# Performance work log

Measured on AMD Instinct MI355X. Metric: run time of the kernel, lower is better.

Reference implementation:

```python
import jax, jax.numpy as jnp
import numpy as np

B, N, C = 1, 256, 128        # batch, n_res, norm_channel
H, AC = 4, 32                # num_head, attention_channel


def setup_inputs() -> dict:
    key = jax.random.key(0)
    ks = jax.random.split(key, 9)
    s = 0.02
    return {
        "act": jax.random.normal(ks[0], (B, N, N, C), jnp.float32),
        "mask": jnp.ones((B, N, N), jnp.float32),
        "ln_g": jnp.ones((C,), jnp.float32),
        "ln_b": jnp.zeros((C,), jnp.float32),
        "wq": (jax.random.normal(ks[1], (C, H * AC), jnp.float32) * s),
        "wk": (jax.random.normal(ks[2], (C, H * AC), jnp.float32) * s),
        "wv": (jax.random.normal(ks[3], (C, H * AC), jnp.float32) * s),
        "w2d": (jax.random.normal(ks[4], (C, H), jnp.float32) * s),
        "wg": (jax.random.normal(ks[5], (C, H * AC), jnp.float32) * s),
        "bg": jnp.zeros((H * AC,), jnp.float32),
        "wo": (jax.random.normal(ks[6], (H * AC, C), jnp.float32) * s),
        "bo": jnp.zeros((C,), jnp.float32),
    }


def reference(act, mask, ln_g, ln_b, wq, wk, wv, w2d, wg, bg, wo, bo):
    eps = 1e-5
    mu = jnp.mean(act, axis=-1, keepdims=True)
    var = jnp.mean(jnp.square(act - mu), axis=-1, keepdims=True)
    a = (act - mu) * jax.lax.rsqrt(var + eps) * ln_g + ln_b  # LayerNorm

    b_, m_, i_, _ = a.shape
    q = (a @ wq).reshape(b_, m_, i_, H, AC)
    k = (a @ wk).reshape(b_, m_, i_, H, AC)
    v = (a @ wv).reshape(b_, m_, i_, H, AC)

    factor = 1.0 / np.sqrt(AC).astype(np.float32)
    # mask bias: [b, m, 1, 1, j]
    bias = (1e9 * (mask - 1.0))[:, :, None, None, :]
    aff = jnp.einsum('bmihc,bmjhc->bmhij', q * factor, k) + bias

    # pair bias: [b, h, i, j], broadcast over m (torch trailing-dim broadcast, b=1)
    nb = jnp.einsum('bijc,ch->bhij', a, w2d)
    weights = jax.nn.softmax(aff + nb[:, None], axis=-1)  # [b,m,h,i,j]

    g = jax.nn.sigmoid(a @ wg + bg).reshape(b_, m_, i_, H, AC)
    out = jnp.einsum('bmhqk,bmkhc->bmqhc', weights, v) * g  # [b,m,q,h,c]
    return out.reshape(b_, m_, i_, H * AC) @ wo + bo
```

## Files before the change

### kernel.cpp

```cpp
#include <hip/hip_runtime.h>
#include <hip/hip_fp16.h>
#include <math.h>


#define NRES 256
#define CCH  128
#define NROWS (NRES * NRES)
#define FACTOR 0.17677669529663687f
#define LOG2E  1.44269504088896341f

typedef __attribute__((ext_vector_type(8))) __bf16 bf16x8;
typedef __attribute__((ext_vector_type(4))) float f32x4;
typedef __attribute__((ext_vector_type(4))) short s16x4;

__device__ __forceinline__ f32x4 mfma16(bf16x8 a, bf16x8 b, f32x4 c) {
    return __builtin_amdgcn_mfma_f32_16x16x32_bf16(a, b, c, 0, 0, 0);
}
__device__ __forceinline__ f32x4 mfma16x16(s16x4 a, s16x4 b, f32x4 c) {
    return __builtin_amdgcn_mfma_f32_16x16x16bf16_1k(a, b, c, 0, 0, 0);
}

union PK4 { __bf16 b[4]; uint2 u2; s16x4 s4; };

__device__ __forceinline__ void hilo(float x, __bf16& h, __bf16& l) {
    h = (__bf16)x;
    l = (__bf16)(x - (float)h);
}

__global__ __launch_bounds__(256) void pre_kernel(
    const float* __restrict__ act, const float* __restrict__ ln_g,
    const float* __restrict__ ln_b, const float* __restrict__ w2d,
    const float* __restrict__ wq, const float* __restrict__ wk,
    const float* __restrict__ wv, const float* __restrict__ wg,
    const float* __restrict__ wo,
    __bf16* __restrict__ wph, __bf16* __restrict__ wo16h,
    __bf16* __restrict__ wo16l,
    float* __restrict__ nbP, __bf16* __restrict__ aLN)
{
    const int t = threadIdx.x;
    if (blockIdx.x >= 2048) {
        const int gid = (blockIdx.x - 2048) * 256 + t;
        const int wid = gid >> 11;
        const int rem = gid & 2047;
        const int lane = rem & 63;
        const int l15 = lane & 15, quad = lane >> 4;
        if (wid < 4) {
            const int nstrip = rem >> 8;
            const int kf = (rem >> 6) & 3;
            const float* W = (wid == 0) ? wq : (wid == 1) ? wk :
                             (wid == 2) ? wv : wg;
            const float scale = (wid == 0) ? FACTOR * LOG2E : 1.0f;
            bf16x8 hb;
            #pragma unroll
            for (int e = 0; e < 8; ++e) {
                int k = kf * 32 + quad * 8 + e;
                int n = nstrip * 16 + l15;
                hb[e] = (__bf16)(W[k * CCH + n] * scale);
            }
            *(bf16x8*)&wph[(size_t)gid * 8] = hb;
        } else {
            const int nstrip = rem >> 8;
            const int kcp = (rem >> 6) & 3;
            #pragma unroll
            for (int sub = 0; sub < 2; ++sub) {
                const int kc = kcp * 2 + sub;
                PK4 hh, ll;
                #pragma unroll
                for (int e = 0; e < 4; ++e) {
                    int k = kc * 16 + quad * 4 + e;
                    int n = nstrip * 16 + l15;
                    __bf16 h, l; hilo(wo[k * CCH + n], h, l);
                    hh.b[e] = h; ll.b[e] = l;
                }
                const int fo = ((nstrip * 8 + kc) * 64 + lane) * 4;
                *(uint2*)&wo16h[fo] = hh.u2;
                *(uint2*)&wo16l[fo] = ll.u2;
            }
        }
        return;
    }
    const int ridx = t >> 3, g = t & 7;
    const int grow = blockIdx.x * 32 + ridx;
    const float* __restrict__ xp = act + (size_t)grow * CCH + g * 16;
    float4 x4[4];
    #pragma unroll
    for (int c = 0; c < 4; ++c) x4[c] = *(const float4*)(xp + c * 4);
    float s = 0.f, sq = 0.f;
    #pragma unroll
    for (int c = 0; c < 4; ++c) {
        s  += (x4[c].x + x4[c].y) + (x4[c].z + x4[c].w);
        sq += x4[c].x * x4[c].x + x4[c].y * x4[c].y +
              x4[c].z * x4[c].z + x4[c].w * x4[c].w;
    }
    #pragma unroll
    for (int o = 1; o <= 4; o <<= 1) {
        s  += __shfl_xor(s, o, 64);
        sq += __shfl_xor(sq, o, 64);
    }
    float mu  = s * (1.0f / CCH);
    float var = fmaf(sq, 1.0f / CCH, -mu * mu);
    float rs  = rsqrtf(var + 1e-5f);
    float av[16];
    #pragma unroll
    for (int c = 0; c < 4; ++c) {
        float4 g4 = *(const float4*)&ln_g[g * 16 + c * 4];
        float4 b4 = *(const float4*)&ln_b[g * 16 + c * 4];
        float* xv = (float*)&x4[c];
        float* gv = (float*)&g4;
        float* bv = (float*)&b4;
        #pragma unroll
        for (int e = 0; e < 4; ++e)
            av[c * 4 + e] = fmaf((xv[e] - mu) * rs, gv[e], bv[e]);
    }
    bf16x8 o1, o2;
    #pragma unroll
    for (int e = 0; e < 8; ++e) {
        o1[e] = (__bf16)av[e];
        o2[e] = (__bf16)av[8 + e];
    }
    *(bf16x8*)&aLN[(size_t)grow * CCH + g * 16] = o1;
    *(bf16x8*)&aLN[(size_t)grow * CCH + g * 16 + 8] = o2;

    float nb[4] = {0.f, 0.f, 0.f, 0.f};
    const float4* __restrict__ w2d4 = (const float4*)w2d;
    #pragma unroll
    for (int c = 0; c < 16; ++c) {
        float4 wv = w2d4[g * 16 + c];
        nb[0] = fmaf(av[c], wv.x, nb[0]);
        nb[1] = fmaf(av[c], wv.y, nb[1]);
        nb[2] = fmaf(av[c], wv.z, nb[2]);
        nb[3] = fmaf(av[c], wv.w, nb[3]);
    }
    #pragma unroll
    for (int o = 1; o <= 4; o <<= 1)
        #pragma unroll
        for (int hh = 0; hh < 4; ++hh)
            nb[hh] += __shfl_xor(nb[hh], o, 64);
    if (g == 0) {
        const int i = grow >> 8, j = grow & 255;
        #pragma unroll
        for (int hh = 0; hh < 4; ++hh) {
            size_t f = ((size_t)hh << 14) + ((size_t)(i >> 4) << 10) +
                       ((size_t)(j >> 4) << 6) + ((size_t)((j >> 2) & 3) << 4) +
                       (i & 15);
            nbP[f * 4 + (j & 3)] = nb[hh] * LOG2E;
        }
    }
}

__device__ __forceinline__ void proj16(const bf16x8* A0,
    const __bf16* __restrict__ Bh, int lane, f32x4* acc)
{
    #pragma unroll
    for (int n = 0; n < 8; ++n) acc[n] = (f32x4){0.f, 0.f, 0.f, 0.f};
    #pragma unroll
    for (int kf = 0; kf < 4; ++kf)
        #pragma unroll
        for (int n = 0; n < 8; ++n) {
            bf16x8 bh = *(const bf16x8*)&Bh[(size_t)((n * 4 + kf) * 64 + lane) * 8];
            acc[n] = mfma16(A0[kf], bh, acc[n]);
        }
}

__global__ __launch_bounds__(1024) void mega_kernel(
    const __bf16* __restrict__ aLN, const __bf16* __restrict__ wph,
    const __bf16* __restrict__ wo16h, const __bf16* __restrict__ wo16l,
    const float* __restrict__ bg, const float* __restrict__ mask,
    const float* __restrict__ nbP, const float* __restrict__ bo,
    float* __restrict__ out)
{
    __shared__ __align__(16) char smem[138240];
    const int t = threadIdx.x, w = t >> 6, lane = t & 63;
    const int l15 = lane & 15, quad = lane >> 4;
    const int m = blockIdx.x;
    __bf16* const Kl = (__bf16*)smem;
    __bf16* const aH = (__bf16*)(smem + w * 4352);
    __bf16* const VT = (__bf16*)(smem + 69632);
    float*  const biasrow = (float*)(smem + 137216);

    if (t < 256)
        biasrow[t] = fmaf(1.442695e9f, mask[m * NRES + t] - 1.0f, -4.0f * LOG2E);

    bf16x8 A0[4];
    {
        const __bf16* __restrict__ ap =
            aLN + ((size_t)m * NRES + w * 16 + l15) * CCH;
        #pragma unroll
        for (int kf = 0; kf < 4; ++kf)
            A0[kf] = *(const bf16x8*)&ap[kf * 32 + quad * 8];
    }

    f32x4 acc[8];
    bf16x8 Qh[4];
    uint2  greg[4][2];

    proj16(A0, wph, lane, acc);
    {
        __bf16* const sth = aH;
        #pragma unroll
        for (int n = 0; n < 8; ++n)
            #pragma unroll
            for (int r = 0; r < 4; ++r)
                sth[(quad * 4 + r) * 136 + n * 16 + l15] = (__bf16)acc[n][r];
        #pragma unroll
        for (int h = 0; h < 4; ++h)
            Qh[h] = *(const bf16x8*)&sth[l15 * 136 + h * 32 + quad * 8];
    }

    proj16(A0, wph + 3 * 16384, lane, acc);
    {
        __half* const sthH = (__half*)aH;
        #pragma unroll
        for (int n = 0; n < 8; ++n)
            #pragma unroll
            for (int r = 0; r < 4; ++r) {
                float v = acc[n][r] + bg[n * 16 + l15];
                sthH[(quad * 4 + r) * 136 + n * 16 + l15] =
                    (__half)(1.0f / (1.0f + __expf(-v)));
            }
        #pragma unroll
        for (int h = 0; h < 4; ++h)
            #pragma unroll
            for (int c = 0; c < 2; ++c)
                greg[h][c] =
                    *(const uint2*)&sthH[l15 * 136 + h * 32 + c * 16 + quad * 4];
    }

    proj16(A0, wph + 1 * 16384, lane, acc);
    #pragma unroll
    for (int n = 0; n < 8; ++n)
        #pragma unroll
        for (int r = 0; r < 4; ++r)
            aH[(quad * 4 + r) * 136 + n * 16 + l15] = (__bf16)acc[n][r];

    proj16(A0, wph + 2 * 16384, lane, acc);
    {
        const int jcol = w * 16 + quad * 4;
        #pragma unroll
        for (int n = 0; n < 8; ++n) {
            PK4 pv;
            #pragma unroll
            for (int r = 0; r < 4; ++r) pv.b[r] = (__bf16)acc[n][r];
            *(uint2*)&VT[(n * 16 + l15) * 264 + jcol] = pv.u2;
        }
    }

    __syncthreads();

    PK4 ovh[4][2], ovl[4][2];
    #pragma unroll
    for (int h = 0; h < 4; ++h) {
        f32x4 O[2];
        O[0] = (f32x4){0.f, 0.f, 0.f, 0.f};
        O[1] = (f32x4){0.f, 0.f, 0.f, 0.f};
        float ls = 0.f;
        const int nbbase = (h * 16384 + w * 1024 + quad * 16 + l15) * 4;
        #pragma unroll 1
        for (int jb = 0; jb < NRES; jb += 64) {
            bf16x8 Kh[4];
            #pragma unroll
            for (int u = 0; u < 4; ++u)
                Kh[u] = *(const bf16x8*)&Kl[(jb + u * 16 + l15) * 136 +
                                            h * 32 + quad * 8];
            PK4 Vf[2][4];
            #pragma unroll
            for (int c = 0; c < 2; ++c)
                #pragma unroll
                for (int u = 0; u < 4; ++u)
                    Vf[c][u].u2 = *(const uint2*)&VT[
                        (h * 32 + c * 16 + l15) * 264 + jb + u * 16 + quad * 4];
            float4 nb4[4];
            #pragma unroll
            for (int u = 0; u < 4; ++u)
                nb4[u] = *(const float4*)(nbP + nbbase +
                                          (((jb >> 4) + u) << 8));
            f32x4 S[4];
            #pragma unroll
            for (int u = 0; u < 4; ++u) {
                S[u] = (f32x4){0.f, 0.f, 0.f, 0.f};
                S[u] = mfma16(Kh[u], Qh[h], S[u]);
            }
            PK4 PJ[4];
            #pragma unroll
            for (int u = 0; u < 4; ++u) {
                float4 mb = *(const float4*)&biasrow[jb + u * 16 + quad * 4];
                float p0 = exp2f(S[u][0] + nb4[u].x + mb.x);
                float p1 = exp2f(S[u][1] + nb4[u].y + mb.y);
                float p2 = exp2f(S[u][2] + nb4[u].z + mb.z);
                float p3 = exp2f(S[u][3] + nb4[u].w + mb.w);
                ls += (p0 + p1) + (p2 + p3);
                PJ[u].b[0] = (__bf16)p0; PJ[u].b[1] = (__bf16)p1;
                PJ[u].b[2] = (__bf16)p2; PJ[u].b[3] = (__bf16)p3;
            }
            #pragma unroll
            for (int c = 0; c < 2; ++c)
                #pragma unroll
                for (int u = 0; u < 4; ++u)
                    O[c] = mfma16x16(Vf[c][u].s4, PJ[u].s4, O[c]);
        }
        ls += __shfl_xor(ls, 16, 64);
        ls += __shfl_xor(ls, 32, 64);
        float inv = 1.0f / ls;
        #pragma unroll
        for (int c = 0; c < 2; ++c) {
            const __half* gh = (const __half*)&greg[h][c];
            #pragma unroll
            for (int r = 0; r < 4; ++r) {
                float v = O[c][r] * inv * (float)gh[r];
                __bf16 hb; __bf16 lb; hilo(v, hb, lb);
                ovh[h][c].b[r] = hb; ovl[h][c].b[r] = lb;
            }
        }
    }

    {
        #pragma unroll
        for (int n = 0; n < 8; ++n) acc[n] = (f32x4){0.f, 0.f, 0.f, 0.f};
        #pragma unroll
        for (int kc = 0; kc < 8; ++kc) {
            const int h = kc >> 1, c = kc & 1;
            s16x4 Ah = ovh[h][c].s4;
            s16x4 Al = ovl[h][c].s4;
            #pragma unroll
            for (int n = 0; n < 8; ++n) {
                const int fo = ((n * 8 + kc) * 64 + lane) * 4;
                PK4 bh, bl;
                bh.u2 = *(const uint2*)&wo16h[fo];
                bl.u2 = *(const uint2*)&wo16l[fo];
                acc[n] = mfma16x16(Ah, bh.s4, acc[n]);
                acc[n] = mfma16x16(Ah, bl.s4, acc[n]);
                acc[n] = mfma16x16(Al, bh.s4, acc[n]);
            }
        }

        const size_t rbase = (size_t)m * NRES + w * 16;
        #pragma unroll
        for (int n = 0; n < 8; ++n) {
            float b = bo[n * 16 + l15];
            #pragma unroll
            for (int r = 0; r < 4; ++r)
                out[(rbase + quad * 4 + r) * CCH + n * 16 + l15] = acc[n][r] + b;
        }
    }
}

extern "C" void kernel_launch(void* const* d_in, const int* in_sizes, int n_in,
                              void* d_out, int out_size, void* d_ws, size_t ws_size,
                              hipStream_t stream)
{
    const float* act  = (const float*)d_in[0];
    const float* mask = (const float*)d_in[1];
    const float* ln_g = (const float*)d_in[2];
    const float* ln_b = (const float*)d_in[3];
    const float* wq   = (const float*)d_in[4];
    const float* wk   = (const float*)d_in[5];
    const float* wv   = (const float*)d_in[6];
    const float* w2d  = (const float*)d_in[7];
    const float* wg   = (const float*)d_in[8];
    const float* bg   = (const float*)d_in[9];
    const float* wo   = (const float*)d_in[10];
    const float* bo   = (const float*)d_in[11];
    float* out = (float*)d_out;

    float* nbP    = (float*)d_ws;
    __bf16* wph   = (__bf16*)(nbP + 4 * NROWS);
    __bf16* wo16h = wph + 4 * 16384;
    __bf16* wo16l = wo16h + 16384;
    __bf16* aLN   = wo16l + 16384;

    pre_kernel<<<2088, 256, 0, stream>>>(
        act, ln_g, ln_b, w2d, wq, wk, wv, wg, wo, wph, wo16h, wo16l, nbP, aLN);
    mega_kernel<<<256, 1024, 0, stream>>>(
        aLN, wph, wo16h, wo16l, bg, mask, nbP, bo, out);
}
```

Baseline: 188.7 us.

## Fuse LayerNorm and pair-bias into mega kernel with grid-wide atomic barrier

Moves the LayerNorm and pair-bias projection out of the pre-kernel and into the main kernel. Each block normalizes its own 256 rows straight into shared memory, so the bf16 activation buffer no longer has to be written to and re-read from global memory. Because the pair bias for row m is read by every block, each block publishes its nbP slice and increments a global counter, then spins until all 256 blocks have arrived before starting attention. This relies on all 256 blocks being co-resident at once, otherwise it deadlocks, and the prep kernel shrinks to weight conversion only.

```diff
diff --git a/kernel.cpp b/kernel.cpp
--- a/kernel.cpp
+++ b/kernel.cpp
@@ -27,123 +27,51 @@
     l = (__bf16)(x - (float)h);
 }
 
-__global__ __launch_bounds__(256) void pre_kernel(
-    const float* __restrict__ act, const float* __restrict__ ln_g,
-    const float* __restrict__ ln_b, const float* __restrict__ w2d,
+__global__ __launch_bounds__(256) void prep_kernel(
     const float* __restrict__ wq, const float* __restrict__ wk,
     const float* __restrict__ wv, const float* __restrict__ wg,
     const float* __restrict__ wo,
     __bf16* __restrict__ wph, __bf16* __restrict__ wo16h,
-    __bf16* __restrict__ wo16l,
-    float* __restrict__ nbP, __bf16* __restrict__ aLN)
+    __bf16* __restrict__ wo16l, unsigned* __restrict__ cnt)
 {
     const int t = threadIdx.x;
-    if (blockIdx.x >= 2048) {
-        const int gid = (blockIdx.x - 2048) * 256 + t;
-        const int wid = gid >> 11;
-        const int rem = gid & 2047;
-        const int lane = rem & 63;
-        const int l15 = lane & 15, quad = lane >> 4;
-        if (wid < 4) {
-            const int nstrip = rem >> 8;
-            const int kf = (rem >> 6) & 3;
-            const float* W = (wid == 0) ? wq : (wid == 1) ? wk :
-                             (wid == 2) ? wv : wg;
-            const float scale = (wid == 0) ? FACTOR * LOG2E : 1.0f;
-            bf16x8 hb;
-            #pragma unroll
-            for (int e = 0; e < 8; ++e) {
-                int k = kf * 32 + quad * 8 + e;
+    if (blockIdx.x == 0 && t == 0) *cnt = 0;
+    const int gid = blockIdx.x * 256 + t;
+    const int wid = gid >> 11;
+    const int rem = gid & 2047;
+    const int lane = rem & 63;
+    const int l15 = lane & 15, quad = lane >> 4;
+    if (wid < 4) {
+        const int nstrip = rem >> 8;
+        const int kf = (rem >> 6) & 3;
+        const float* W = (wid == 0) ? wq : (wid == 1) ? wk :
+                         (wid == 2) ? wv : wg;
+        const float scale = (wid == 0) ? FACTOR * LOG2E : 1.0f;
+        bf16x8 hb;
+        #pragma unroll
+        for (int e = 0; e < 8; ++e) {
+            int k = kf * 32 + quad * 8 + e;
+            int n = nstrip * 16 + l15;
+            hb[e] = (__bf16)(W[k * CCH + n] * scale);
+        }
+        *(bf16x8*)&wph[(size_t)gid * 8] = hb;
+    } else {
+        const int nstrip = rem >> 8;
+        const int kcp = (rem >> 6) & 3;
+        #pragma unroll
+        for (int sub = 0; sub < 2; ++sub) {
+            const int kc = kcp * 2 + sub;
+            PK4 hh, ll;
+            #pragma unroll
+            for (int e = 0; e < 4; ++e) {
+                int k = kc * 16 + quad * 4 + e;
                 int n = nstrip * 16 + l15;
-                hb[e] = (__bf16)(W[k * CCH + n] * scale);
-            }
-            *(bf16x8*)&wph[(size_t)gid * 8] = hb;
-        } else {
-            const int nstrip = rem >> 8;
-            const int kcp = (rem >> 6) & 3;
-            #pragma unroll
-            for (int sub = 0; sub < 2; ++sub) {
-                const int kc = kcp * 2 + sub;
-                PK4 hh, ll;
-                #pragma unroll
-                for (int e = 0; e < 4; ++e) {
-                    int k = kc * 16 + quad * 4 + e;
-                    int n = nstrip * 16 + l15;
-                    __bf16 h, l; hilo(wo[k * CCH + n], h, l);
-                    hh.b[e] = h; ll.b[e] = l;
-                }
-                const int fo = ((nstrip * 8 + kc) * 64 + lane) * 4;
-                *(uint2*)&wo16h[fo] = hh.u2;
-                *(uint2*)&wo16l[fo] = ll.u2;
-            }
-        }
-        return;
-    }
-    const int ridx = t >> 3, g = t & 7;
-    const int grow = blockIdx.x * 32 + ridx;
-    const float* __restrict__ xp = act + (size_t)grow * CCH + g * 16;
-    float4 x4[4];
-    #pragma unroll
-    for (int c = 0; c < 4; ++c) x4[c] = *(const float4*)(xp + c * 4);
-    float s = 0.f, sq = 0.f;
-    #pragma unroll
-    for (int c = 0; c < 4; ++c) {
-        s  += (x4[c].x + x4[c].y) + (x4[c].z + x4[c].w);
-        sq += x4[c].x * x4[c].x + x4[c].y * x4[c].y +
-              x4[c].z * x4[c].z + x4[c].w * x4[c].w;
-    }
-    #pragma unroll
-    for (int o = 1; o <= 4; o <<= 1) {
-        s  += __shfl_xor(s, o, 64);
-        sq += __shfl_xor(sq, o, 64);
-    }
-    float mu  = s * (1.0f / CCH);
-    float var = fmaf(sq, 1.0f / CCH, -mu * mu);
-    float rs  = rsqrtf(var + 1e-5f);
-    float av[16];
-    #pragma unroll
-    for (int c = 0; c < 4; ++c) {
-        float4 g4 = *(const float4*)&ln_g[g * 16 + c * 4];
-        float4 b4 = *(const float4*)&ln_b[g * 16 + c * 4];
-        float* xv = (float*)&x4[c];
-        float* gv = (float*)&g4;
-        float* bv = (float*)&b4;
-        #pragma unroll
-        for (int e = 0; e < 4; ++e)
-            av[c * 4 + e] = fmaf((xv[e] - mu) * rs, gv[e], bv[e]);
-    }
-    bf16x8 o1, o2;
-    #pragma unroll
-    for (int e = 0; e < 8; ++e) {
-        o1[e] = (__bf16)av[e];
-        o2[e] = (__bf16)av[8 + e];
-    }
-    *(bf16x8*)&aLN[(size_t)grow * CCH + g * 16] = o1;
-    *(bf16x8*)&aLN[(size_t)grow * CCH + g * 16 + 8] = o2;
-
-    float nb[4] = {0.f, 0.f, 0.f, 0.f};
-    const float4* __restrict__ w2d4 = (const float4*)w2d;
-    #pragma unroll
-    for (int c = 0; c < 16; ++c) {
-        float4 wv = w2d4[g * 16 + c];
-        nb[0] = fmaf(av[c], wv.x, nb[0]);
-        nb[1] = fmaf(av[c], wv.y, nb[1]);
-        nb[2] = fmaf(av[c], wv.z, nb[2]);
-        nb[3] = fmaf(av[c], wv.w, nb[3]);
-    }
-    #pragma unroll
-    for (int o = 1; o <= 4; o <<= 1)
-        #pragma unroll
-        for (int hh = 0; hh < 4; ++hh)
-            nb[hh] += __shfl_xor(nb[hh], o, 64);
-    if (g == 0) {
-        const int i = grow >> 8, j = grow & 255;
-        #pragma unroll
-        for (int hh = 0; hh < 4; ++hh) {
-            size_t f = ((size_t)hh << 14) + ((size_t)(i >> 4) << 10) +
-                       ((size_t)(j >> 4) << 6) + ((size_t)((j >> 2) & 3) << 4) +
-                       (i & 15);
-            nbP[f * 4 + (j & 3)] = nb[hh] * LOG2E;
+                __bf16 h, l; hilo(wo[k * CCH + n], h, l);
+                hh.b[e] = h; ll.b[e] = l;
+            }
+            const int fo = ((nstrip * 8 + kc) * 64 + lane) * 4;
+            *(uint2*)&wo16h[fo] = hh.u2;
+            *(uint2*)&wo16l[fo] = ll.u2;
         }
     }
 }
@@ -163,10 +91,12 @@
 }
 
 __global__ __launch_bounds__(1024) void mega_kernel(
-    const __bf16* __restrict__ aLN, const __bf16* __restrict__ wph,
-    const __bf16* __restrict__ wo16h, const __bf16* __restrict__ wo16l,
-    const float* __restrict__ bg, const float* __restrict__ mask,
-    const float* __restrict__ nbP, const float* __restrict__ bo,
+    const float* __restrict__ act, const float* __restrict__ ln_g,
+    const float* __restrict__ ln_b, const float* __restrict__ w2d,
+    const __bf16* __restrict__ wph, const __bf16* __restrict__ wo16h,
+    const __bf16* __restrict__ wo16l, const float* __restrict__ bg,
+    const float* __restrict__ mask, float* __restrict__ nbP,
+    const float* __restrict__ bo, unsigned* __restrict__ cnt,
     float* __restrict__ out)
 {
     __shared__ __align__(16) char smem[138240];
@@ -181,14 +111,78 @@
     if (t < 256)
         biasrow[t] = fmaf(1.442695e9f, mask[m * NRES + t] - 1.0f, -4.0f * LOG2E);
 
+    {
+        const int row = lane >> 2, gq = lane & 3;
+        const int grow = m * NRES + w * 16 + row;
+        const float* __restrict__ xp = act + (size_t)grow * CCH + gq * 32;
+        float4 x4[8];
+        #pragma unroll
+        for (int c = 0; c < 8; ++c) x4[c] = *(const float4*)(xp + c * 4);
+        float s = 0.f, sq = 0.f;
+        #pragma unroll
+        for (int c = 0; c < 8; ++c) {
+            s  += (x4[c].x + x4[c].y) + (x4[c].z + x4[c].w);
+            sq += x4[c].x * x4[c].x + x4[c].y * x4[c].y +
+                  x4[c].z * x4[c].z + x4[c].w * x4[c].w;
+        }
+        #pragma unroll
+        for (int o = 1; o <= 2; o <<= 1) {
+            s  += __shfl_xor(s, o, 64);
+            sq += __shfl_xor(sq, o, 64);
+        }
+        float mu  = s * (1.0f / CCH);
+        float var = fmaf(sq, 1.0f / CCH, -mu * mu);
+        float rs  = rsqrtf(var + 1e-5f);
+        float nb[4] = {0.f, 0.f, 0.f, 0.f};
+        const float4* __restrict__ w2d4 = (const float4*)w2d;
+        #pragma unroll
+        for (int c2 = 0; c2 < 4; ++c2) {
+            bf16x8 pk;
+            #pragma unroll
+            for (int cc = 0; cc < 2; ++cc) {
+                const int c = c2 * 2 + cc;
+                float4 g4 = *(const float4*)&ln_g[gq * 32 + c * 4];
+                float4 b4 = *(const float4*)&ln_b[gq * 32 + c * 4];
+                float* xv = (float*)&x4[c];
+                float* gv = (float*)&g4;
+                float* bv = (float*)&b4;
+                #pragma unroll
+                for (int e = 0; e < 4; ++e) {
+                    float av = fmaf((xv[e] - mu) * rs, gv[e], bv[e]);
+                    pk[cc * 4 + e] = (__bf16)av;
+                    float4 wv = w2d4[gq * 32 + c * 4 + e];
+                    nb[0] = fmaf(av, wv.x, nb[0]);
+                    nb[1] = fmaf(av, wv.y, nb[1]);
+                    nb[2] = fmaf(av, wv.z, nb[2]);
+                    nb[3] = fmaf(av, wv.w, nb[3]);
+                }
+            }
+            *(bf16x8*)&aH[row * 136 + gq * 32 + c2 * 8] = pk;
+        }
+        #pragma unroll
+        for (int o = 1; o <= 2; o <<= 1)
+            #pragma unroll
+            for (int hh = 0; hh < 4; ++hh)
+                nb[hh] += __shfl_xor(nb[hh], o, 64);
+        if (gq == 0) {
+            const int j = w * 16 + row;
+            #pragma unroll
+            for (int hh = 0; hh < 4; ++hh) {
+                int f = (hh << 14) + ((m >> 4) << 10) + ((j >> 4) << 6) +
+                        (((j >> 2) & 3) << 4) + (m & 15);
+                nbP[f * 4 + (j & 3)] = nb[hh] * LOG2E;
+            }
+        }
+    }
+    __syncthreads();
+    if (t == 0)
+        __hip_atomic_fetch_add(cnt, 1u, __ATOMIC_RELEASE,
+                               __HIP_MEMORY_SCOPE_AGENT);
+
     bf16x8 A0[4];
-    {
-        const __bf16* __restrict__ ap =
-            aLN + ((size_t)m * NRES + w * 16 + l15) * CCH;
-        #pragma unroll
-        for (int kf = 0; kf < 4; ++kf)
-            A0[kf] = *(const bf16x8*)&ap[kf * 32 + quad * 8];
-    }
+    #pragma unroll
+    for (int kf = 0; kf < 4; ++kf)
+        A0[kf] = *(const bf16x8*)&aH[l15 * 136 + kf * 32 + quad * 8];
 
     f32x4 acc[8];
     bf16x8 Qh[4];
@@ -245,6 +239,10 @@
         }
     }
 
+    __syncthreads();
+    if (t == 0)
+        while (__hip_atomic_load(cnt, __ATOMIC_ACQUIRE,
+                                 __HIP_MEMORY_SCOPE_AGENT) < 256u) {}
     __syncthreads();
 
     PK4 ovh[4][2], ovl[4][2];
@@ -366,10 +364,10 @@
     __bf16* wph   = (__bf16*)(nbP + 4 * NROWS);
     __bf16* wo16h = wph + 4 * 16384;
     __bf16* wo16l = wo16h + 16384;
-    __bf16* aLN   = wo16l + 16384;
-
-    pre_kernel<<<2088, 256, 0, stream>>>(
-        act, ln_g, ln_b, w2d, wq, wk, wv, wg, wo, wph, wo16h, wo16l, nbP, aLN);
+    unsigned* cnt = (unsigned*)(wo16l + 16384);
+
+    prep_kernel<<<40, 256, 0, stream>>>(
+        wq, wk, wv, wg, wo, wph, wo16h, wo16l, cnt);
     mega_kernel<<<256, 1024, 0, stream>>>(
-        aLN, wph, wo16h, wo16l, bg, mask, nbP, bo, out);
-}
+        act, ln_g, ln_b, w2d, wph, wo16h, wo16l, bg, mask, nbP, bo, cnt, out);
+}
```

Measured after the change: 193.8 us. 1.03x slower.
